# Optimization experiments

Hardware: AMD Instinct MI355X
Metric: run time of the kernel (lower is better)

Reference implementation:

```python
import jax, jax.numpy as jnp
import numpy as np

H, DM, LQ, LK, DK, DV = 16, 1024, 2048, 2048, 64, 64
B = 2

def setup_inputs() -> dict:
    key = jax.random.key(0)
    ks = jax.random.split(key, 12)
    s = 0.02  # init scale for weights
    return {
        "Q": jax.random.normal(ks[0], (B, LQ, DM), jnp.float32),
        "K": jax.random.normal(ks[1], (B, LK, DM), jnp.float32),
        "V": jax.random.normal(ks[2], (B, LK, DM), jnp.float32),
        "mask": jax.random.randint(ks[3], (B, LQ), 0, 2, jnp.int32),
        "W_Q": jax.random.normal(ks[4], (H * DK, DM), jnp.float32) * s,
        "b_Q": jnp.zeros((H * DK,), jnp.float32),
        "W_K": jax.random.normal(ks[5], (H * DK, DM), jnp.float32) * s,
        "b_K": jnp.zeros((H * DK,), jnp.float32),
        "W_V": jax.random.normal(ks[6], (H * DV, DM), jnp.float32) * s,
        "b_V": jnp.zeros((H * DV,), jnp.float32),
        "W_O": jax.random.normal(ks[7], (DM, H * DV), jnp.float32) * s,
        "b_O": jnp.zeros((DM,), jnp.float32),
    }

def reference(Q, K, V, mask, W_Q, b_Q, W_K, b_K, W_V, b_V, W_O, b_O):
    b = Q.shape[0]
    q = (Q @ W_Q.T + b_Q).reshape(b, LQ, H, DK)
    k = (K @ W_K.T + b_K).reshape(b, LK, H, DK)
    v = (V @ W_V.T + b_V).reshape(b, LK, H, DV)
    # scores: [b, h, q, k]
    A = jnp.einsum('bqhd,bkhd->bhqk', q, k) / jnp.sqrt(jnp.float32(DK))
    # mask masks whole QUERY rows; softmax is over the query axis (dim=1 in torch's [B*h, lq, lk])
    A = jnp.where(mask[:, None, :, None] == 0, -jnp.inf, A)
    alpha = jax.nn.softmax(A, axis=2)  # over query axis, per original masked branch
    out = jnp.einsum('bhqk,bkhd->bqhd', alpha, v).reshape(b, LQ, H * DV)
    return out @ W_O.T + b_O + Q  # output proj + residual
```

## Files before the change

kernel.cpp:

```cpp
#include <hip/hip_runtime.h>
#include <hip/hip_bf16.h>
#include <stdint.h>

using frag8 = __attribute__((ext_vector_type(8))) short;
using f32x4 = __attribute__((ext_vector_type(4))) float;

#define MFMA16 __builtin_amdgcn_mfma_f32_16x16x32_bf16

#if __has_builtin(__builtin_amdgcn_exp2f)
#define EXP2F(x) __builtin_amdgcn_exp2f(x)
#else
#define EXP2F(x) __expf((x) * 0.6931471805599453f)
#endif
#if __has_builtin(__builtin_amdgcn_rcpf)
#define RCPF(x) __builtin_amdgcn_rcpf(x)
#else
#define RCPF(x) (1.0f / (x))
#endif

#define SCALE_Q 0.18033688011112042f

__device__ __forceinline__ short f2bf(float f) {
    union { float f; uint32_t u; } x; x.f = f;
    uint32_t r = x.u + 0x7fffu + ((x.u >> 16) & 1u);
    return (short)(r >> 16);
}
__device__ __forceinline__ float bf2f(short s) {
    union { uint32_t u; float f; } x; x.u = ((uint32_t)(uint16_t)s) << 16;
    return x.f;
}
__device__ __forceinline__ uint32_t pack2bf(float a, float b) {
    float2 t; t.x = a; t.y = b;
    __hip_bfloat162 h = __float22bfloat162_rn(t);
    union { __hip_bfloat162 h; uint32_t u; } c; c.h = h;
    return c.u;
}
__device__ __forceinline__ frag8 cvt8(float4 a, float4 b) {
    frag8 r;
    r[0] = f2bf(a.x); r[1] = f2bf(a.y); r[2] = f2bf(a.z); r[3] = f2bf(a.w);
    r[4] = f2bf(b.x); r[5] = f2bf(b.y); r[6] = f2bf(b.z); r[7] = f2bf(b.w);
    return r;
}
__device__ __forceinline__ frag8 addbf8(uint4 x, uint4 y) {
    frag8 r;
    const ushort* xs = (const ushort*)&x;
    const ushort* ys = (const ushort*)&y;
#pragma unroll
    for (int i = 0; i < 8; i++)
        r[i] = f2bf(bf2f((short)xs[i]) + bf2f((short)ys[i]));
    return r;
}

__global__ __launch_bounds__(64) void k_compact(const int* __restrict__ mask,
                                                int* __restrict__ idx,
                                                int* __restrict__ nU) {
    const int b = blockIdx.x, ln = threadIdx.x;
    const int* m = mask + b * 2048;
    int* id = idx + b * 2048;
    int base = 0;
    for (int c = 0; c < 32; c++) {
        int i = c * 64 + ln;
        int mv = m[i];
        unsigned long long bal = __ballot(mv != 0);
        int rank = __popcll(bal & ((1ull << ln) - 1ull));
        if (mv) id[base + rank] = i;
        base += __popcll(bal);
    }
    if (ln == 0) nU[b] = base;
    int nUr = (base + 63) & ~63;
    for (int i = base + ln; i < nUr; i += 64) id[i] = 0;
}

__global__ __launch_bounds__(256) void k_zero2(uint4* __restrict__ a,
                                               uint4* __restrict__ b, int n16) {
    int i = blockIdx.x * 256 + threadIdx.x;
    if (i < n16) { uint4 z = {0, 0, 0, 0}; a[i] = z; b[i] = z; }
}

__global__ __launch_bounds__(256) void k_psum(short* __restrict__ p0,
                                              const short* __restrict__ p1, int n8) {
    int i = blockIdx.x * 256 + threadIdx.x;
    int st = gridDim.x * 256;
    for (; i < n8; i += st) {
        uint4 a = ((const uint4*)p0)[i];
        uint4 b = ((const uint4*)p1)[i];
        frag8 r = addbf8(a, b);
        ((uint4*)p0)[i] = *(uint4*)&r;
    }
}

__global__ __launch_bounds__(256) void k_gather(const short* __restrict__ q_s,
                                                const int* __restrict__ idx,
                                                const int* __restrict__ nU,
                                                short* __restrict__ q_c) {
    const int bh = blockIdx.x, tile = blockIdx.y, b = bh >> 4;
    const int n = nU[b], nUr = (n + 63) & ~63;
    const int i = tile * 64 + (threadIdx.x >> 2);
    if (i >= nUr) return;
    const int src = idx[b * 2048 + i];
    const uint4* sp = (const uint4*)(q_s + ((size_t)bh * 2048 + src) * 64);
    uint4* dp = (uint4*)(q_c + ((size_t)bh * 2048 + i) * 64);
    const int c = threadIdx.x & 3;
    dp[c] = sp[c];
    dp[c + 4] = sp[c + 4];
}

__global__ __launch_bounds__(256) void k_cvt_w(
    const float* __restrict__ s0, const float* __restrict__ s1,
    const float* __restrict__ s2, const float* __restrict__ s3,
    short* __restrict__ d0, short* __restrict__ d1,
    short* __restrict__ d2, short* __restrict__ d3) {
    const int W4 = 262144;
    int i = blockIdx.x * 256 + threadIdx.x;
    int st = gridDim.x * 256;
    for (; i < 4 * W4; i += st) {
        int seg = i / W4, j = i - seg * W4;
        const float* sp = seg == 0 ? s0 : seg == 1 ? s1 : seg == 2 ? s2 : s3;
        short* dp = seg == 0 ? d0 : seg == 1 ? d1 : seg == 2 ? d2 : d3;
        float4 v = ((const float4*)sp)[j];
        ushort4 o;
        o.x = (uint16_t)f2bf(v.x); o.y = (uint16_t)f2bf(v.y);
        o.z = (uint16_t)f2bf(v.z); o.w = (uint16_t)f2bf(v.w);
        ((ushort4*)dp)[j] = o;
    }
}

__device__ __forceinline__ void stage64x128(const short* __restrict__ g, int rs,
                                            short* lds, int tid) {
#pragma unroll
    for (int j = 0; j < 2; j++) {
        int chunk = j * 256 + tid;
        int row = chunk >> 3, c = chunk & 7;
        int sc = c ^ (row & 7);
        __builtin_amdgcn_global_load_lds(
            (const __attribute__((address_space(1))) uint32_t*)(g + (size_t)row * rs + sc * 8),
            (__attribute__((address_space(3))) uint32_t*)(lds + (j * 256 + (tid & 192)) * 8),
            16, 0, 0);
    }
}
__device__ __forceinline__ frag8 ldswz(const short* lds, int row, int cc) {
    return *(const frag8*)(lds + row * 64 + ((cc ^ (row & 7)) << 3));
}

__device__ __forceinline__ void stage_tiles(const short* __restrict__ As,
                                            const short* __restrict__ Bs,
                                            short* lA, short* lB,
                                            int w, int ln) {
#pragma unroll
    for (int j = 0; j < 2; j++) {
        int cb = (w * 2 + j) * 64;
        int c  = cb + ln;
        int row = c >> 2, c8 = c & 3;
        __builtin_amdgcn_global_load_lds(
            (const __attribute__((address_space(1))) uint32_t*)(As + row * 1024 + c8 * 8),
            (__attribute__((address_space(3))) uint32_t*)(lA + cb * 8), 16, 0, 0);
        __builtin_amdgcn_global_load_lds(
            (const __attribute__((address_space(1))) uint32_t*)(Bs + row * 1024 + c8 * 8),
            (__attribute__((address_space(3))) uint32_t*)(lB + cb * 8), 16, 0, 0);
    }
}
__device__ __forceinline__ void stage_b(const short* __restrict__ Bs,
                                        short* lB, int w, int ln) {
#pragma unroll
    for (int j = 0; j < 2; j++) {
        int cb = (w * 2 + j) * 64;
        int c  = cb + ln;
        int row = c >> 2, c8 = c & 3;
        __builtin_amdgcn_global_load_lds(
            (const __attribute__((address_space(1))) uint32_t*)(Bs + row * 1024 + c8 * 8),
            (__attribute__((address_space(3))) uint32_t*)(lB + cb * 8), 16, 0, 0);
    }
}

__global__ __launch_bounds__(256) void k_proj3(
    const float* __restrict__ A0, const float* __restrict__ A1, const float* __restrict__ A2,
    const short* __restrict__ B0, const short* __restrict__ B1, const short* __restrict__ B2,
    const float* __restrict__ bias0, const float* __restrict__ bias1, const float* __restrict__ bias2,
    short* __restrict__ dst0, short* __restrict__ dst1, short* __restrict__ dst2) {
    __shared__ short lA[2][4096];
    __shared__ short lB[2][4096];
    const int wg = blockIdx.x;
    const int tmlow = wg & 7, tnb = (wg >> 3) & 7, rest = wg >> 6;
    const int tmh = rest & 3, z = rest >> 2;
    const int tmb = tmlow | (tmh << 3);
    const float* A  = z == 0 ? A0 : z == 1 ? A1 : A2;
    const short* Bt = z == 0 ? B0 : z == 1 ? B1 : B2;
    const float* bias = z == 0 ? bias0 : z == 1 ? bias1 : bias2;
    short* dst = z == 0 ? dst0 : z == 1 ? dst1 : dst2;
    const float scale = z == 0 ? SCALE_Q : 1.0f;

    const int tid = threadIdx.x, w = tid >> 6, ln = tid & 63;
    const int wm = w >> 1, wn = w & 1, r16 = ln & 15, g = ln >> 4;
    const int tn = tnb * 128, tm = tmb * 128;
    const float* Ab = A + (size_t)tm * 1024;
    const short* Bb = Bt + (size_t)tn * 1024;

    const int cb0 = (w * 2 + 0) * 64 + ln, cb1 = (w * 2 + 1) * 64 + ln;
    const int rA0 = cb0 >> 2, cA0 = cb0 & 3, rA1 = cb1 >> 2, cA1 = cb1 & 3;

    float4 ra[4];
    f32x4 acc[4][4] = {};

    {
        const float* a0 = Ab + (size_t)rA0 * 1024 + cA0 * 8;
        ra[0] = *(const float4*)a0; ra[1] = *(const float4*)(a0 + 4);
        const float* a1 = Ab + (size_t)rA1 * 1024 + cA1 * 8;
        ra[2] = *(const float4*)a1; ra[3] = *(const float4*)(a1 + 4);
    }
    stage_b(Bb, &lB[0][0], w, ln);
    *(frag8*)&lA[0][cb0 * 8] = cvt8(ra[0], ra[1]);
    *(frag8*)&lA[0][cb1 * 8] = cvt8(ra[2], ra[3]);

    int buf = 0;
    for (int ks = 0; ks < 32; ks++) {
        if (ks + 1 < 32) {
            const float* a0 = Ab + (size_t)rA0 * 1024 + (ks + 1) * 32 + cA0 * 8;
            ra[0] = *(const float4*)a0; ra[1] = *(const float4*)(a0 + 4);
            const float* a1 = Ab + (size_t)rA1 * 1024 + (ks + 1) * 32 + cA1 * 8;
            ra[2] = *(const float4*)a1; ra[3] = *(const float4*)(a1 + 4);
        }
        __syncthreads();
        if (ks + 1 < 32)
            stage_b(Bb + (ks + 1) * 32, &lB[buf ^ 1][0], w, ln);
        frag8 af[4], bg[4];
#pragma unroll
        for (int mf = 0; mf < 4; mf++)
            af[mf] = *(const frag8*)&lA[buf][(wm * 64 + mf * 16 + r16) * 32 + g * 8];
#pragma unroll
        for (int nf = 0; nf < 4; nf++)
            bg[nf] = *(const frag8*)&lB[buf][(wn * 64 + nf * 16 + r16) * 32 + g * 8];
#pragma unroll
        for (int mf = 0; mf < 4; mf++)
#pragma unroll
            for (int nf = 0; nf < 4; nf++)
                acc[mf][nf] = MFMA16(af[mf], bg[nf], acc[mf][nf], 0, 0, 0);
        if (ks + 1 < 32) {
            *(frag8*)&lA[buf ^ 1][cb0 * 8] = cvt8(ra[0], ra[1]);
            *(frag8*)&lA[buf ^ 1][cb1 * 8] = cvt8(ra[2], ra[3]);
        }
        buf ^= 1;
    }
#pragma unroll
    for (int mf = 0; mf < 4; mf++)
#pragma unroll
        for (int nf = 0; nf < 4; nf++)
#pragma unroll
            for (int r = 0; r < 4; r++) {
                int m = tm + wm * 64 + mf * 16 + g * 4 + r;
                int n = tn + wn * 64 + nf * 16 + r16;
                float val = (acc[mf][nf][r] + bias[n]) * scale;
                int b = m >> 11, seq = m & 2047, h = n >> 6, d = n & 63;
                dst[((size_t)(b * 16 + h) * 2048 + seq) * 64 + d] = f2bf(val);
            }
}

__global__ __launch_bounds__(256, 3) void k_stats(const short* __restrict__ k_s,
                                                  const short* __restrict__ q_c,
                                                  const int* __restrict__ nU,
                                                  const short* __restrict__ v_s,
                                                  short* __restrict__ vhatT) {
    __shared__ short lQ[2][4096];
    __shared__ float lD[128];
    __shared__ short lT[128 * 70];
    const int wg = blockIdx.x;
    const int x = wg & 7, r2 = wg >> 3;
    const int kt = r2 & 15;
    const int bh = x + 8 * (r2 >> 4);
    const int b = bh >> 4;
    const int n = nU[b], nUr = (n + 63) & ~63;
    const int tid = threadIdx.x, w = tid >> 6, ln = tid & 63;
    const int r16 = ln & 15, g = ln >> 4;
    const int kbase = kt * 128 + w * 32;

    const short* kp = k_s + ((size_t)bh * 2048 + kbase) * 64;
    frag8 kf[2][2];
#pragma unroll
    for (int mfk = 0; mfk < 2; mfk++)
#pragma unroll
        for (int kk = 0; kk < 2; kk++)
            kf[mfk][kk] = *(const frag8*)(kp + (mfk * 16 + r16) * 64 + kk * 32 + g * 8);

    const short* qsp = q_c + (size_t)bh * 2048 * 64;
    float dacc[2][4] = {};
    const f32x4 z4 = {0.f, 0.f, 0.f, 0.f};

    if (nUr > 0) {
        stage64x128(qsp, 64, &lQ[0][0], tid);
        int buf = 0;
        for (int qb = 0; qb < nUr; qb += 64) {
            __syncthreads();
            if (qb + 64 < nUr)
                stage64x128(qsp + (size_t)(qb + 64) * 64, 64, &lQ[buf ^ 1][0], tid);
            const short* Qc = &lQ[buf][0];
#pragma unroll
            for (int nf = 0; nf < 4; nf++) {
                float fm = (qb + nf * 16 + r16 < n) ? 1.0f : 0.0f;
                frag8 bq0 = ldswz(Qc, nf * 16 + r16, g);
                frag8 bq1 = ldswz(Qc, nf * 16 + r16, 4 + g);
#pragma unroll
                for (int mfk = 0; mfk < 2; mfk++) {
                    f32x4 s = MFMA16(kf[mfk][0], bq0, z4, 0, 0, 0);
                    s = MFMA16(kf[mfk][1], bq1, s, 0, 0, 0);
#pragma unroll
                    for (int r = 0; r < 4; r++)
                        dacc[mfk][r] += fm * EXP2F(s[r]);
                }
            }
            buf ^= 1;
        }
    }
#pragma unroll
    for (int mfk = 0; mfk < 2; mfk++)
#pragma unroll
        for (int r = 0; r < 4; r++) {
            float v = dacc[mfk][r];
#pragma unroll
            for (int off = 1; off < 16; off <<= 1)
                v += __shfl_xor(v, off, 16);
            dacc[mfk][r] = v;
        }
    if (r16 == 0) {
#pragma unroll
        for (int mfk = 0; mfk < 2; mfk++)
#pragma unroll
            for (int r = 0; r < 4; r++)
                lD[w * 32 + mfk * 16 + g * 4 + r] = RCPF(dacc[mfk][r]);
    }
    const short* vrow = v_s + ((size_t)bh * 2048 + kt * 128) * 64;
#pragma unroll
    for (int i = 0; i < 8; i++) {
        int idx4 = i * 256 + tid;
        int row = idx4 >> 4, c4 = idx4 & 15;
        uint2 u = *(const uint2*)(vrow + (size_t)row * 64 + c4 * 4);
        *(uint32_t*)&lT[row * 70 + c4 * 4]     = u.x;
        *(uint32_t*)&lT[row * 70 + c4 * 4 + 2] = u.y;
    }
    __syncthreads();
    {
        int d = tid >> 2, kc = tid & 3;
        short* dstp = vhatT + ((size_t)bh * 64 + d) * 2048 + kt * 128 + kc * 32;
        uint32_t wd[16];
#pragma unroll
        for (int j2 = 0; j2 < 16; j2++) {
            int k0 = kc * 32 + j2 * 2;
            float v0 = bf2f(lT[k0 * 70 + d]) * lD[k0];
            float v1 = bf2f(lT[(k0 + 1) * 70 + d]) * lD[k0 + 1];
            wd[j2] = pack2bf(v0, v1);
        }
#pragma unroll
        for (int j4 = 0; j4 < 4; j4++) {
            uint4 o = {wd[j4 * 4], wd[j4 * 4 + 1], wd[j4 * 4 + 2], wd[j4 * 4 + 3]};
            *((uint4*)dstp + j4) = o;
        }
    }
}

__global__ __launch_bounds__(256, 3) void k_apply(const short* __restrict__ q_c,
                                                  const short* __restrict__ k_s,
                                                  const short* __restrict__ vhatT,
                                                  const int* __restrict__ idx,
                                                  const int* __restrict__ nU,
                                                  short* __restrict__ p0,
                                                  short* __restrict__ p1) {
    __shared__ short lK[2][4096];
    __shared__ short lV[2][4096];
    __shared__ short lP[128 * 64];
    const int wg = blockIdx.x;
    const int x = wg & 7, r2 = wg >> 3;
    const int qt = r2 & 15, y = r2 >> 4;
    const int bhsp = (y << 3) | x;
    const int bh = bhsp >> 1, sp = bhsp & 1;
    const int b = bh >> 4, h = bh & 15;
    const int n = nU[b];
    if (qt * 128 >= n) return;
    const int tid = threadIdx.x, w = tid >> 6, ln = tid & 63;
    const int r16 = ln & 15, g = ln >> 4;

    const short* qp = q_c + ((size_t)bh * 2048 + qt * 128 + w * 32) * 64;
    frag8 qf[2][2];
#pragma unroll
    for (int qi = 0; qi < 2; qi++)
#pragma unroll
        for (int kk = 0; kk < 2; kk++)
            qf[qi][kk] = *(const frag8*)(qp + (qi * 16 + r16) * 64 + kk * 32 + g * 8);

    const short* kp = k_s + ((size_t)bh * 2048 + sp * 1024) * 64;
    const short* vp = vhatT + (size_t)bh * 64 * 2048 + sp * 1024;

    f32x4 oacc[2][4] = {};
    const f32x4 z4 = {0.f, 0.f, 0.f, 0.f};

    stage64x128(kp, 64, &lK[0][0], tid);
    stage64x128(vp, 2048, &lV[0][0], tid);
    int buf = 0;
    for (int kb = 0; kb < 1024; kb += 64) {
        __syncthreads();
        if (kb + 64 < 1024) {
            stage64x128(kp + (size_t)(kb + 64) * 64, 64, &lK[buf ^ 1][0], tid);
            stage64x128(vp + kb + 64, 2048, &lV[buf ^ 1][0], tid);
        }
        const short* Kc = &lK[buf][0];
        const short* Vc = &lV[buf][0];
        frag8 vb[4][2];
#pragma unroll
        for (int nf = 0; nf < 4; nf++)
#pragma unroll
            for (int kk = 0; kk < 2; kk++)
                vb[nf][kk] = ldswz(Vc, nf * 16 + r16, kk * 4 + g);
#pragma unroll
        for (int qi = 0; qi < 2; qi++) {
            const int prow = w * 32 + qi * 16 + r16;
            const int rx = prow & 7;
#pragma unroll
            for (int mf2 = 0; mf2 < 4; mf2++) {
                f32x4 s = z4;
#pragma unroll
                for (int kk = 0; kk < 2; kk++)
                    s = MFMA16(ldswz(Kc, mf2 * 16 + r16, kk * 4 + g), qf[qi][kk], s, 0, 0, 0);
                float e0 = EXP2F(s[0]), e1 = EXP2F(s[1]);
                float e2 = EXP2F(s[2]), e3 = EXP2F(s[3]);
                uint2 pk;
                pk.x = pack2bf(e0, e1);
                pk.y = pack2bf(e2, e3);
                int o = mf2 * 32 + g * 8;
                int addr = prow * 128 + (((o >> 4) ^ rx) << 4) + (o & 15);
                *(uint2*)((char*)lP + addr) = pk;
            }
        }
#pragma unroll
        for (int qi = 0; qi < 2; qi++) {
            const int prow = w * 32 + qi * 16 + r16;
            const int rx = prow & 7;
            frag8 pa[2];
#pragma unroll
            for (int kk = 0; kk < 2; kk++)
                pa[kk] = *(const frag8*)((char*)lP + prow * 128 + (((kk * 4 + g) ^ rx) << 4));
#pragma unroll
            for (int nf = 0; nf < 4; nf++)
#pragma unroll
                for (int kk = 0; kk < 2; kk++)
                    oacc[qi][nf] = MFMA16(pa[kk], vb[nf][kk], oacc[qi][nf], 0, 0, 0);
        }
        buf ^= 1;
    }
    short* op = sp ? p1 : p0;
#pragma unroll
    for (int qi = 0; qi < 2; qi++)
#pragma unroll
        for (int r = 0; r < 4; r++) {
            int lq = qt * 128 + w * 32 + qi * 16 + g * 4 + r;
            if (lq < n) {
                int qg = idx[b * 2048 + lq];
#pragma unroll
                for (int nf = 0; nf < 4; nf++) {
                    int d = nf * 16 + r16;
                    op[((size_t)(b * 2048 + qg)) * 1024 + h * 64 + d] = f2bf(oacc[qi][nf][r]);
                }
            }
        }
}

__global__ __launch_bounds__(256) void k_final(const short* __restrict__ A,
                                               const short* __restrict__ Bt,
                                               const float* __restrict__ bias,
                                               const float* __restrict__ Qres,
                                               float* __restrict__ out) {
    __shared__ short lA[2][4096];
    __shared__ short lB[2][4096];
    const int wg = blockIdx.x;
    const int tmb = (wg & 7) | ((wg >> 6) << 3);
    const int tnb = (wg >> 3) & 7;
    const int tid = threadIdx.x, w = tid >> 6, ln = tid & 63;
    const int wm = w >> 1, wn = w & 1, r16 = ln & 15, g = ln >> 4;
    const int tn = tnb * 128, tm = tmb * 128;
    const short* Ab = A + (size_t)tm * 1024;
    const short* Bb = Bt + (size_t)tn * 1024;

    f32x4 acc[4][4] = {};
    stage_tiles(Ab, Bb, &lA[0][0], &lB[0][0], w, ln);
    int buf = 0;
    for (int ks = 0; ks < 32; ks++) {
        __syncthreads();
        if (ks + 1 < 32)
            stage_tiles(Ab + (ks + 1) * 32, Bb + (ks + 1) * 32,
                        &lA[buf ^ 1][0], &lB[buf ^ 1][0], w, ln);
        frag8 af[4], bg[4];
#pragma unroll
        for (int mf = 0; mf < 4; mf++)
            af[mf] = *(const frag8*)&lA[buf][(wm * 64 + mf * 16 + r16) * 32 + g * 8];
#pragma unroll
        for (int nf = 0; nf < 4; nf++)
            bg[nf] = *(const frag8*)&lB[buf][(wn * 64 + nf * 16 + r16) * 32 + g * 8];
#pragma unroll
        for (int mf = 0; mf < 4; mf++)
#pragma unroll
            for (int nf = 0; nf < 4; nf++)
                acc[mf][nf] = MFMA16(af[mf], bg[nf], acc[mf][nf], 0, 0, 0);
        buf ^= 1;
    }
#pragma unroll
    for (int mf = 0; mf < 4; mf++)
#pragma unroll
        for (int nf = 0; nf < 4; nf++)
#pragma unroll
            for (int r = 0; r < 4; r++) {
                int m = tm + wm * 64 + mf * 16 + g * 4 + r;
                int n = tn + wn * 64 + nf * 16 + r16;
                float val = acc[mf][nf][r] + bias[n] + Qres[(size_t)m * 1024 + n];
                out[(size_t)m * 1024 + n] = val;
            }
}

extern "C" void kernel_launch(void* const* d_in, const int* in_sizes, int n_in,
                              void* d_out, int out_size, void* d_ws, size_t ws_size,
                              hipStream_t stream) {
    (void)in_sizes; (void)n_in; (void)out_size; (void)ws_size;
    const float* Qf  = (const float*)d_in[0];
    const float* Kf  = (const float*)d_in[1];
    const float* Vf  = (const float*)d_in[2];
    const int*   msk = (const int*)d_in[3];
    const float* WQ  = (const float*)d_in[4];
    const float* bQ  = (const float*)d_in[5];
    const float* WK  = (const float*)d_in[6];
    const float* bK  = (const float*)d_in[7];
    const float* WV  = (const float*)d_in[8];
    const float* bV  = (const float*)d_in[9];
    const float* WO  = (const float*)d_in[10];
    const float* bO  = (const float*)d_in[11];
    float* out = (float*)d_out;

    char* p = (char*)d_ws;
    const size_t SZ_ACT = (size_t)4096 * 1024 * 2;
    const size_t SZ_W   = (size_t)1024 * 1024 * 2;
    short* q_s   = (short*)p; p += SZ_ACT;
    short* k_s   = (short*)p; p += SZ_ACT;
    short* v_s   = (short*)p; p += SZ_ACT;
    short* vhatT = (short*)p; p += SZ_ACT;
    short* p0    = (short*)p; p += SZ_ACT;
    short* q_c   = (short*)p; p += SZ_ACT;
    short* Wqb = (short*)p; p += SZ_W;
    short* Wkb = (short*)p; p += SZ_W;
    short* Wvb = (short*)p; p += SZ_W;
    short* Wob = (short*)p; p += SZ_W;
    int* idx = (int*)p; p += (size_t)2 * 2048 * 4;
    int* nU  = (int*)p; p += 256;
    short* p1 = v_s;

    k_compact<<<2, 64, 0, stream>>>(msk, idx, nU);

    k_cvt_w<<<1024, 256, 0, stream>>>(WQ, WK, WV, WO, Wqb, Wkb, Wvb, Wob);

    k_proj3<<<768, 256, 0, stream>>>(Qf, Kf, Vf, Wqb, Wkb, Wvb,
                                     bQ, bK, bV, q_s, k_s, v_s);

    k_gather<<<dim3(32, 32), 256, 0, stream>>>(q_s, idx, nU, q_c);

    k_stats<<<512, 256, 0, stream>>>(k_s, q_c, nU, v_s, vhatT);

    k_zero2<<<2048, 256, 0, stream>>>((uint4*)p0, (uint4*)p1, 524288);

    k_apply<<<1024, 256, 0, stream>>>(q_c, k_s, vhatT, idx, nU, p0, p1);

    k_psum<<<2048, 256, 0, stream>>>(p0, p1, 524288);

    k_final<<<256, 256, 0, stream>>>(p0, Wob, bO, Qf, out);
}
```

Measured before the change: 161.5 us.

## Fuse query gather into projection scatter and partial-sum into final GEMM

Compaction now also computes an inverse permutation, so the Q projection writes unmasked rows directly into compacted order and the separate gather kernel is dropped. The partial-sum kernel is removed; the final GEMM loads both bf16 partial buffers and adds them while staging A into LDS. Q/K/V activations are pre-converted to bf16 in one combined conversion kernel with the weights, so the projection can use async global-to-LDS loads. This trades two launches and their traffic for an extra full activation conversion pass and register-prefetch staging in the final GEMM.

```diff
diff --git a/kernel.cpp b/kernel.cpp
--- a/kernel.cpp
+++ b/kernel.cpp
@@ -21,9 +21,9 @@
 #define SCALE_Q 0.18033688011112042f
 
 __device__ __forceinline__ short f2bf(float f) {
-    union { float f; uint32_t u; } x; x.f = f;
-    uint32_t r = x.u + 0x7fffu + ((x.u >> 16) & 1u);
-    return (short)(r >> 16);
+    union { __hip_bfloat16 h; short s; } c;
+    c.h = __float2bfloat16(f);
+    return c.s;
 }
 __device__ __forceinline__ float bf2f(short s) {
     union { uint32_t u; float f; } x; x.u = ((uint32_t)(uint16_t)s) << 16;
@@ -35,40 +35,40 @@
     union { __hip_bfloat162 h; uint32_t u; } c; c.h = h;
     return c.u;
 }
-__device__ __forceinline__ frag8 cvt8(float4 a, float4 b) {
-    frag8 r;
-    r[0] = f2bf(a.x); r[1] = f2bf(a.y); r[2] = f2bf(a.z); r[3] = f2bf(a.w);
-    r[4] = f2bf(b.x); r[5] = f2bf(b.y); r[6] = f2bf(b.z); r[7] = f2bf(b.w);
-    return r;
-}
-__device__ __forceinline__ frag8 addbf8(uint4 x, uint4 y) {
-    frag8 r;
-    const ushort* xs = (const ushort*)&x;
-    const ushort* ys = (const ushort*)&y;
-#pragma unroll
-    for (int i = 0; i < 8; i++)
-        r[i] = f2bf(bf2f((short)xs[i]) + bf2f((short)ys[i]));
-    return r;
+__device__ __forceinline__ uint32_t addpk(uint32_t a, uint32_t b) {
+    float a0 = bf2f((short)(a & 0xffff)), a1 = bf2f((short)(a >> 16));
+    float b0 = bf2f((short)(b & 0xffff)), b1 = bf2f((short)(b >> 16));
+    return pack2bf(a0 + b0, a1 + b1);
+}
+__device__ __forceinline__ frag8 add8(uint4 x, uint4 y) {
+    union { uint32_t u[4]; frag8 f; } r;
+    r.u[0] = addpk(x.x, y.x); r.u[1] = addpk(x.y, y.y);
+    r.u[2] = addpk(x.z, y.z); r.u[3] = addpk(x.w, y.w);
+    return r.f;
 }
 
 __global__ __launch_bounds__(64) void k_compact(const int* __restrict__ mask,
                                                 int* __restrict__ idx,
+                                                int* __restrict__ invp,
                                                 int* __restrict__ nU) {
     const int b = blockIdx.x, ln = threadIdx.x;
     const int* m = mask + b * 2048;
-    int* id = idx + b * 2048;
-    int base = 0;
+    int tot = 0;
+    for (int c = 0; c < 32; c++)
+        tot += __popcll(__ballot(m[c * 64 + ln] != 0));
+    int base = 0, mbase = tot;
     for (int c = 0; c < 32; c++) {
         int i = c * 64 + ln;
         int mv = m[i];
         unsigned long long bal = __ballot(mv != 0);
         int rank = __popcll(bal & ((1ull << ln) - 1ull));
-        if (mv) id[base + rank] = i;
-        base += __popcll(bal);
-    }
-    if (ln == 0) nU[b] = base;
-    int nUr = (base + 63) & ~63;
-    for (int i = base + ln; i < nUr; i += 64) id[i] = 0;
+        int nb = __popcll(bal);
+        int pos = mv ? (base + rank) : (mbase + ln - rank);
+        invp[b * 2048 + i] = pos;
+        if (mv) idx[b * 2048 + pos] = i;
+        base += nb; mbase += 64 - nb;
+    }
+    if (ln == 0) nU[b] = tot;
 }
 
 __global__ __launch_bounds__(256) void k_zero2(uint4* __restrict__ a,
@@ -77,51 +77,33 @@
     if (i < n16) { uint4 z = {0, 0, 0, 0}; a[i] = z; b[i] = z; }
 }
 
-__global__ __launch_bounds__(256) void k_psum(short* __restrict__ p0,
-                                              const short* __restrict__ p1, int n8) {
+__global__ __launch_bounds__(256) void k_cvt_all(
+    const float* __restrict__ s0, const float* __restrict__ s1,
+    const float* __restrict__ s2, const float* __restrict__ s3,
+    const float* __restrict__ s4, const float* __restrict__ s5,
+    const float* __restrict__ s6,
+    short* __restrict__ d0, short* __restrict__ d1, short* __restrict__ d2,
+    short* __restrict__ d3, short* __restrict__ d4, short* __restrict__ d5,
+    short* __restrict__ d6) {
+    const int A4 = 1048576, W4 = 262144;
     int i = blockIdx.x * 256 + threadIdx.x;
     int st = gridDim.x * 256;
-    for (; i < n8; i += st) {
-        uint4 a = ((const uint4*)p0)[i];
-        uint4 b = ((const uint4*)p1)[i];
-        frag8 r = addbf8(a, b);
-        ((uint4*)p0)[i] = *(uint4*)&r;
-    }
-}
-
-__global__ __launch_bounds__(256) void k_gather(const short* __restrict__ q_s,
-                                                const int* __restrict__ idx,
-                                                const int* __restrict__ nU,
-                                                short* __restrict__ q_c) {
-    const int bh = blockIdx.x, tile = blockIdx.y, b = bh >> 4;
-    const int n = nU[b], nUr = (n + 63) & ~63;
-    const int i = tile * 64 + (threadIdx.x >> 2);
-    if (i >= nUr) return;
-    const int src = idx[b * 2048 + i];
-    const uint4* sp = (const uint4*)(q_s + ((size_t)bh * 2048 + src) * 64);
-    uint4* dp = (uint4*)(q_c + ((size_t)bh * 2048 + i) * 64);
-    const int c = threadIdx.x & 3;
-    dp[c] = sp[c];
-    dp[c + 4] = sp[c + 4];
-}
-
-__global__ __launch_bounds__(256) void k_cvt_w(
-    const float* __restrict__ s0, const float* __restrict__ s1,
-    const float* __restrict__ s2, const float* __restrict__ s3,
-    short* __restrict__ d0, short* __restrict__ d1,
-    short* __restrict__ d2, short* __restrict__ d3) {
-    const int W4 = 262144;
-    int i = blockIdx.x * 256 + threadIdx.x;
-    int st = gridDim.x * 256;
-    for (; i < 4 * W4; i += st) {
-        int seg = i / W4, j = i - seg * W4;
-        const float* sp = seg == 0 ? s0 : seg == 1 ? s1 : seg == 2 ? s2 : s3;
-        short* dp = seg == 0 ? d0 : seg == 1 ? d1 : seg == 2 ? d2 : d3;
-        float4 v = ((const float4*)sp)[j];
-        ushort4 o;
-        o.x = (uint16_t)f2bf(v.x); o.y = (uint16_t)f2bf(v.y);
-        o.z = (uint16_t)f2bf(v.z); o.w = (uint16_t)f2bf(v.w);
-        ((ushort4*)dp)[j] = o;
+    const int total = 3 * A4 + 4 * W4;
+    for (; i < total; i += st) {
+        const float* s; short* d; int j;
+        if (i < A4)            { s = s0; d = d0; j = i; }
+        else if (i < 2 * A4)   { s = s1; d = d1; j = i - A4; }
+        else if (i < 3 * A4)   { s = s2; d = d2; j = i - 2 * A4; }
+        else {
+            int t = i - 3 * A4; int seg = t / W4; j = t - seg * W4;
+            s = seg == 0 ? s3 : seg == 1 ? s4 : seg == 2 ? s5 : s6;
+            d = seg == 0 ? d3 : seg == 1 ? d4 : seg == 2 ? d5 : d6;
+        }
+        float4 v = reinterpret_cast<const float4*>(s)[j];
+        uint2 o;
+        o.x = pack2bf(v.x, v.y);
+        o.y = pack2bf(v.z, v.w);
+        reinterpret_cast<uint2*>(d)[j] = o;
     }
 }
 
@@ -173,9 +155,10 @@
 }
 
 __global__ __launch_bounds__(256) void k_proj3(
-    const float* __restrict__ A0, const float* __restrict__ A1, const float* __restrict__ A2,
+    const short* __restrict__ A0, const short* __restrict__ A1, const short* __restrict__ A2,
     const short* __restrict__ B0, const short* __restrict__ B1, const short* __restrict__ B2,
     const float* __restrict__ bias0, const float* __restrict__ bias1, const float* __restrict__ bias2,
+    const int* __restrict__ invp,
     short* __restrict__ dst0, short* __restrict__ dst1, short* __restrict__ dst2) {
     __shared__ short lA[2][4096];
     __shared__ short lB[2][4096];
@@ -183,7 +166,7 @@
     const int tmlow = wg & 7, tnb = (wg >> 3) & 7, rest = wg >> 6;
     const int tmh = rest & 3, z = rest >> 2;
     const int tmb = tmlow | (tmh << 3);
-    const float* A  = z == 0 ? A0 : z == 1 ? A1 : A2;
+    const short* A  = z == 0 ? A0 : z == 1 ? A1 : A2;
     const short* Bt = z == 0 ? B0 : z == 1 ? B1 : B2;
     const float* bias = z == 0 ? bias0 : z == 1 ? bias1 : bias2;
     short* dst = z == 0 ? dst0 : z == 1 ? dst1 : dst2;
@@ -192,36 +175,17 @@
     const int tid = threadIdx.x, w = tid >> 6, ln = tid & 63;
     const int wm = w >> 1, wn = w & 1, r16 = ln & 15, g = ln >> 4;
     const int tn = tnb * 128, tm = tmb * 128;
-    const float* Ab = A + (size_t)tm * 1024;
+    const short* Ab = A + (size_t)tm * 1024;
     const short* Bb = Bt + (size_t)tn * 1024;
 
-    const int cb0 = (w * 2 + 0) * 64 + ln, cb1 = (w * 2 + 1) * 64 + ln;
-    const int rA0 = cb0 >> 2, cA0 = cb0 & 3, rA1 = cb1 >> 2, cA1 = cb1 & 3;
-
-    float4 ra[4];
     f32x4 acc[4][4] = {};
-
-    {
-        const float* a0 = Ab + (size_t)rA0 * 1024 + cA0 * 8;
-        ra[0] = *(const float4*)a0; ra[1] = *(const float4*)(a0 + 4);
-        const float* a1 = Ab + (size_t)rA1 * 1024 + cA1 * 8;
-        ra[2] = *(const float4*)a1; ra[3] = *(const float4*)(a1 + 4);
-    }
-    stage_b(Bb, &lB[0][0], w, ln);
-    *(frag8*)&lA[0][cb0 * 8] = cvt8(ra[0], ra[1]);
-    *(frag8*)&lA[0][cb1 * 8] = cvt8(ra[2], ra[3]);
-
+    stage_tiles(Ab, Bb, &lA[0][0], &lB[0][0], w, ln);
     int buf = 0;
     for (int ks = 0; ks < 32; ks++) {
-        if (ks + 1 < 32) {
-            const float* a0 = Ab + (size_t)rA0 * 1024 + (ks + 1) * 32 + cA0 * 8;
-            ra[0] = *(const float4*)a0; ra[1] = *(const float4*)(a0 + 4);
-            const float* a1 = Ab + (size_t)rA1 * 1024 + (ks + 1) * 32 + cA1 * 8;
-            ra[2] = *(const float4*)a1; ra[3] = *(const float4*)(a1 + 4);
-        }
         __syncthreads();
         if (ks + 1 < 32)
-            stage_b(Bb + (ks + 1) * 32, &lB[buf ^ 1][0], w, ln);
+            stage_tiles(Ab + (ks + 1) * 32, Bb + (ks + 1) * 32,
+                        &lA[buf ^ 1][0], &lB[buf ^ 1][0], w, ln);
         frag8 af[4], bg[4];
 #pragma unroll
         for (int mf = 0; mf < 4; mf++)
@@ -234,28 +198,27 @@
 #pragma unroll
             for (int nf = 0; nf < 4; nf++)
                 acc[mf][nf] = MFMA16(af[mf], bg[nf], acc[mf][nf], 0, 0, 0);
-        if (ks + 1 < 32) {
-            *(frag8*)&lA[buf ^ 1][cb0 * 8] = cvt8(ra[0], ra[1]);
-            *(frag8*)&lA[buf ^ 1][cb1 * 8] = cvt8(ra[2], ra[3]);
-        }
         buf ^= 1;
     }
 #pragma unroll
     for (int mf = 0; mf < 4; mf++)
 #pragma unroll
-        for (int nf = 0; nf < 4; nf++)
-#pragma unroll
-            for (int r = 0; r < 4; r++) {
-                int m = tm + wm * 64 + mf * 16 + g * 4 + r;
+        for (int r = 0; r < 4; r++) {
+            int m = tm + wm * 64 + mf * 16 + g * 4 + r;
+            int b = m >> 11, seq = m & 2047;
+            int sq = (z == 0) ? invp[b * 2048 + seq] : seq;
+#pragma unroll
+            for (int nf = 0; nf < 4; nf++) {
                 int n = tn + wn * 64 + nf * 16 + r16;
                 float val = (acc[mf][nf][r] + bias[n]) * scale;
-                int b = m >> 11, seq = m & 2047, h = n >> 6, d = n & 63;
-                dst[((size_t)(b * 16 + h) * 2048 + seq) * 64 + d] = f2bf(val);
+                int h = n >> 6, d = n & 63;
+                dst[((size_t)(b * 16 + h) * 2048 + sq) * 64 + d] = f2bf(val);
             }
+        }
 }
 
 __global__ __launch_bounds__(256, 3) void k_stats(const short* __restrict__ k_s,
-                                                  const short* __restrict__ q_c,
+                                                  const short* __restrict__ q_s,
                                                   const int* __restrict__ nU,
                                                   const short* __restrict__ v_s,
                                                   short* __restrict__ vhatT) {
@@ -280,7 +243,7 @@
         for (int kk = 0; kk < 2; kk++)
             kf[mfk][kk] = *(const frag8*)(kp + (mfk * 16 + r16) * 64 + kk * 32 + g * 8);
 
-    const short* qsp = q_c + (size_t)bh * 2048 * 64;
+    const short* qsp = q_s + (size_t)bh * 2048 * 64;
     float dacc[2][4] = {};
     const f32x4 z4 = {0.f, 0.f, 0.f, 0.f};
 
@@ -355,7 +318,7 @@
     }
 }
 
-__global__ __launch_bounds__(256, 3) void k_apply(const short* __restrict__ q_c,
+__global__ __launch_bounds__(256, 3) void k_apply(const short* __restrict__ q_s,
                                                   const short* __restrict__ k_s,
                                                   const short* __restrict__ vhatT,
                                                   const int* __restrict__ idx,
@@ -376,7 +339,7 @@
     const int tid = threadIdx.x, w = tid >> 6, ln = tid & 63;
     const int r16 = ln & 15, g = ln >> 4;
 
-    const short* qp = q_c + ((size_t)bh * 2048 + qt * 128 + w * 32) * 64;
+    const short* qp = q_s + ((size_t)bh * 2048 + qt * 128 + w * 32) * 64;
     frag8 qf[2][2];
 #pragma unroll
     for (int qi = 0; qi < 2; qi++)
@@ -460,7 +423,8 @@
         }
 }
 
-__global__ __launch_bounds__(256) void k_final(const short* __restrict__ A,
+__global__ __launch_bounds__(256) void k_final(const short* __restrict__ p0,
+                                               const short* __restrict__ p1,
                                                const short* __restrict__ Bt,
                                                const float* __restrict__ bias,
                                                const float* __restrict__ Qres,
@@ -473,17 +437,44 @@
     const int tid = threadIdx.x, w = tid >> 6, ln = tid & 63;
     const int wm = w >> 1, wn = w & 1, r16 = ln & 15, g = ln >> 4;
     const int tn = tnb * 128, tm = tmb * 128;
-    const short* Ab = A + (size_t)tm * 1024;
+    const short* A0 = p0 + (size_t)tm * 1024;
+    const short* A1 = p1 + (size_t)tm * 1024;
     const short* Bb = Bt + (size_t)tn * 1024;
 
+    const int cb0 = (w * 2 + 0) * 64 + ln, cb1 = (w * 2 + 1) * 64 + ln;
+    const int rA0 = cb0 >> 2, cA0 = (cb0 & 3) * 8;
+    const int rA1 = cb1 >> 2, cA1 = (cb1 & 3) * 8;
+
     f32x4 acc[4][4] = {};
-    stage_tiles(Ab, Bb, &lA[0][0], &lB[0][0], w, ln);
+    uint4 ra0, rb0, ra1, rb1;
+
+    {
+        uint4 x0 = *(const uint4*)(A0 + (size_t)rA0 * 1024 + cA0);
+        uint4 y0 = *(const uint4*)(A1 + (size_t)rA0 * 1024 + cA0);
+        uint4 x1 = *(const uint4*)(A0 + (size_t)rA1 * 1024 + cA1);
+        uint4 y1 = *(const uint4*)(A1 + (size_t)rA1 * 1024 + cA1);
+        stage_b(Bb, &lB[0][0], w, ln);
+        *(frag8*)&lA[0][cb0 * 8] = add8(x0, y0);
+        *(frag8*)&lA[0][cb1 * 8] = add8(x1, y1);
+        ra0 = *(const uint4*)(A0 + (size_t)rA0 * 1024 + 32 + cA0);
+        rb0 = *(const uint4*)(A1 + (size_t)rA0 * 1024 + 32 + cA0);
+        ra1 = *(const uint4*)(A0 + (size_t)rA1 * 1024 + 32 + cA1);
+        rb1 = *(const uint4*)(A1 + (size_t)rA1 * 1024 + 32 + cA1);
+    }
     int buf = 0;
     for (int ks = 0; ks < 32; ks++) {
         __syncthreads();
-        if (ks + 1 < 32)
-            stage_tiles(Ab + (ks + 1) * 32, Bb + (ks + 1) * 32,
-                        &lA[buf ^ 1][0], &lB[buf ^ 1][0], w, ln);
+        if (ks + 1 < 32) {
+            *(frag8*)&lA[buf ^ 1][cb0 * 8] = add8(ra0, rb0);
+            *(frag8*)&lA[buf ^ 1][cb1 * 8] = add8(ra1, rb1);
+            stage_b(Bb + (ks + 1) * 32, &lB[buf ^ 1][0], w, ln);
+        }
+        if (ks + 2 < 32) {
+            ra0 = *(const uint4*)(A0 + (size_t)rA0 * 1024 + (ks + 2) * 32 + cA0);
+            rb0 = *(const uint4*)(A1 + (size_t)rA0 * 1024 + (ks + 2) * 32 + cA0);
+            ra1 = *(const uint4*)(A0 + (size_t)rA1 * 1024 + (ks + 2) * 32 + cA1);
+            rb1 = *(const uint4*)(A1 + (size_t)rA1 * 1024 + (ks + 2) * 32 + cA1);
+        }
         frag8 af[4], bg[4];
 #pragma unroll
         for (int mf = 0; mf < 4; mf++)
@@ -532,36 +523,36 @@
     char* p = (char*)d_ws;
     const size_t SZ_ACT = (size_t)4096 * 1024 * 2;
     const size_t SZ_W   = (size_t)1024 * 1024 * 2;
-    short* q_s   = (short*)p; p += SZ_ACT;
-    short* k_s   = (short*)p; p += SZ_ACT;
-    short* v_s   = (short*)p; p += SZ_ACT;
-    short* vhatT = (short*)p; p += SZ_ACT;
-    short* p0    = (short*)p; p += SZ_ACT;
-    short* q_c   = (short*)p; p += SZ_ACT;
+    short* Qb  = (short*)p; p += SZ_ACT;
+    short* Kb  = (short*)p; p += SZ_ACT;
+    short* Vb  = (short*)p; p += SZ_ACT;
+    short* q_s = (short*)p; p += SZ_ACT;
+    short* k_s = (short*)p; p += SZ_ACT;
+    short* v_s = (short*)p; p += SZ_ACT;
     short* Wqb = (short*)p; p += SZ_W;
     short* Wkb = (short*)p; p += SZ_W;
     short* Wvb = (short*)p; p += SZ_W;
     short* Wob = (short*)p; p += SZ_W;
-    int* idx = (int*)p; p += (size_t)2 * 2048 * 4;
-    int* nU  = (int*)p; p += 256;
-    short* p1 = v_s;
-
-    k_compact<<<2, 64, 0, stream>>>(msk, idx, nU);
-
-    k_cvt_w<<<1024, 256, 0, stream>>>(WQ, WK, WV, WO, Wqb, Wkb, Wvb, Wob);
-
-    k_proj3<<<768, 256, 0, stream>>>(Qf, Kf, Vf, Wqb, Wkb, Wvb,
-                                     bQ, bK, bV, q_s, k_s, v_s);
-
-    k_gather<<<dim3(32, 32), 256, 0, stream>>>(q_s, idx, nU, q_c);
-
-    k_stats<<<512, 256, 0, stream>>>(k_s, q_c, nU, v_s, vhatT);
+    int* idx  = (int*)p; p += (size_t)2 * 2048 * 4;
+    int* invp = (int*)p; p += (size_t)2 * 2048 * 4;
+    int* nU   = (int*)p; p += 256;
+    short* vhatT = Qb;
+    short* p0    = Kb;
+    short* p1    = Vb;
+
+    k_compact<<<2, 64, 0, stream>>>(msk, idx, invp, nU);
+
+    k_cvt_all<<<4096, 256, 0, stream>>>(Qf, Kf, Vf, WQ, WK, WV, WO,
+                                        Qb, Kb, Vb, Wqb, Wkb, Wvb, Wob);
+
+    k_proj3<<<768, 256, 0, stream>>>(Qb, Kb, Vb, Wqb, Wkb, Wvb,
+                                     bQ, bK, bV, invp, q_s, k_s, v_s);
+
+    k_stats<<<512, 256, 0, stream>>>(k_s, q_s, nU, v_s, vhatT);
 
     k_zero2<<<2048, 256, 0, stream>>>((uint4*)p0, (uint4*)p1, 524288);
 
-    k_apply<<<1024, 256, 0, stream>>>(q_c, k_s, vhatT, idx, nU, p0, p1);
-
-    k_psum<<<2048, 256, 0, stream>>>(p0, p1, 524288);
-
-    k_final<<<256, 256, 0, stream>>>(p0, Wob, bO, Qf, out);
-}
+    k_apply<<<1024, 256, 0, stream>>>(q_s, k_s, vhatT, idx, nU, p0, p1);
+
+    k_final<<<256, 256, 0, stream>>>(p0, p1, Wob, bO, Qf, out);
+}
```

After: 161.5 us. No clear change (+0.0%).
